# Kernel tuning notes

Measured on AMD Instinct MI355X. Metric: run time of the kernel, lower is better.

Reference implementation:

```python
import jax, jax.numpy as jnp
import numpy as np

N_NODES = 10000
N_EDGES = 4096
IN_F = 300
OUT_F = 150


def setup_inputs() -> dict:
    key = jax.random.key(0)
    ks = jax.random.split(key, 7)
    features = jax.random.normal(ks[0], (N_NODES, IN_F), dtype=jnp.float32)
    efeat = jax.random.normal(ks[1], (N_EDGES, 1), dtype=jnp.float32)
    # edge_func: Linear(1, IN_F*OUT_F) producing per-edge weight matrices
    W_edge = jax.random.normal(ks[2], (1, IN_F * OUT_F), dtype=jnp.float32) * (1.0)
    b_edge = jax.random.normal(ks[3], (IN_F * OUT_F,), dtype=jnp.float32) * 0.02
    bias = jax.random.normal(ks[4], (OUT_F,), dtype=jnp.float32) * 0.02
    src = jax.random.randint(ks[5], (N_EDGES,), 0, N_NODES, dtype=jnp.int32)
    dst = jax.random.randint(ks[6], (N_EDGES,), 0, N_NODES, dtype=jnp.int32)
    return {"features": features, "efeat": efeat, "W_edge": W_edge,
            "b_edge": b_edge, "bias": bias, "src": src, "dst": dst}


def reference(features, efeat, W_edge, b_edge, bias, src, dst):
    # edge_func: Linear on edge features -> per-edge weight matrix [E, IN_F, OUT_F]
    We = (efeat @ W_edge + b_edge).reshape(-1, IN_F, OUT_F)
    # gather source node features and apply per-edge matmul: m_e = h_src[e] @ W_e
    h_src = features[src]                       # [E, IN_F]
    msgs = jnp.einsum('ei,eio->eo', h_src, We)  # [E, OUT_F]
    # scatter-mean to destination nodes
    sums = jax.ops.segment_sum(msgs, dst, num_segments=N_NODES)          # [N, OUT_F]
    cnts = jax.ops.segment_sum(jnp.ones((msgs.shape[0],), msgs.dtype), dst,
                               num_segments=N_NODES)                     # [N]
    mean = sums / jnp.maximum(cnts, 1.0)[:, None]  # nodes w/o in-edges -> 0
    return jax.nn.relu(mean + bias)
```

## Files before the change

### kernel.cpp

```cpp
#include <hip/hip_runtime.h>

#define NNODES 10000
#define NEDGES 4096
#define INF 300
#define OUTF 150
#define EPB 16
#define NGROUPS (NEDGES / EPB)
#define SPLITK 5
#define KCHUNK (INF / SPLITK)
#define PHASES 3
#define PROWS (KCHUNK / PHASES)
#define ETHREADS 192

#define SUMS_N (NNODES * OUTF)

__global__ __launch_bounds__(ETHREADS, 4) void edge_msg_kernel(
    const float* __restrict__ feat, const float* __restrict__ efeat,
    const float* __restrict__ W, const float* __restrict__ B,
    const int* __restrict__ src, const int* __restrict__ dst,
    float* __restrict__ sums, float* __restrict__ cnts)
{
    __shared__ float hA[EPB][KCHUNK];
    __shared__ float s_ef[EPB];
    __shared__ int   s_dst[EPB];
    __shared__ int   s_src[EPB];

    const int tid = threadIdx.x;
    const int kc  = blockIdx.x / NGROUPS;
    const int grp = blockIdx.x - kc * NGROUPS;
    const int e0  = grp * EPB;
    const int k0  = kc * KCHUNK;

    if (tid < EPB) {
        const int e = e0 + tid;
        s_src[tid] = src[e];
        s_dst[tid] = dst[e];
        s_ef[tid]  = efeat[e];
    }
    __syncthreads();

    for (int q = tid; q < EPB * (KCHUNK / 4); q += ETHREADS) {
        const int el = q / (KCHUNK / 4);
        const int j4 = q - el * (KCHUNK / 4);
        *(float4*)&hA[el][4 * j4] =
            *(const float4*)(feat + (size_t)s_src[el] * INF + k0 + 4 * j4);
    }
    __syncthreads();

    if (tid < OUTF) {
        float accW[EPB], accB[EPB];
        #pragma unroll
        for (int e = 0; e < EPB; ++e) { accW[e] = 0.f; accB[e] = 0.f; }

        const float* Wc = W + (size_t)k0 * OUTF + tid;
        const float* Bc = B + (size_t)k0 * OUTF + tid;

        #pragma unroll
        for (int ph = 0; ph < PHASES; ++ph) {
            const int base = ph * PROWS;
            float wr[PROWS], br[PROWS];
            #pragma unroll
            for (int r = 0; r < PROWS; ++r) {
                wr[r] = Wc[(size_t)(base + r) * OUTF];
                br[r] = Bc[(size_t)(base + r) * OUTF];
            }
            #pragma unroll
            for (int i4 = 0; i4 < PROWS; i4 += 4) {
                #pragma unroll
                for (int e = 0; e < EPB; ++e) {
                    const float4 h = *(const float4*)&hA[e][base + i4];
                    accW[e] = fmaf(h.w, wr[i4 + 3], fmaf(h.z, wr[i4 + 2],
                              fmaf(h.y, wr[i4 + 1], fmaf(h.x, wr[i4 + 0], accW[e]))));
                    accB[e] = fmaf(h.w, br[i4 + 3], fmaf(h.z, br[i4 + 2],
                              fmaf(h.y, br[i4 + 1], fmaf(h.x, br[i4 + 0], accB[e]))));
                }
            }
        }
        #pragma unroll
        for (int e = 0; e < EPB; ++e) {
            const float msg = fmaf(s_ef[e], accW[e], accB[e]);
            atomicAdd(&sums[(size_t)s_dst[e] * OUTF + tid], msg);
        }
    } else if (kc == 0 && tid < OUTF + EPB) {
        atomicAdd(&cnts[s_dst[tid - OUTF]], 1.0f);
    }
}

__global__ __launch_bounds__(256) void finalize_kernel(
    const float* __restrict__ sums, const float* __restrict__ cnts,
    const float* __restrict__ bias, float* __restrict__ out)
{
    const int idx = blockIdx.x * blockDim.x + threadIdx.x;
    if (idx < SUMS_N) {
        const int n = idx / OUTF;
        const int o = idx - n * OUTF;
        const float c = cnts[n];
        const float m = sums[idx] / fmaxf(c, 1.0f);
        const float v = m + bias[o];
        out[idx] = v > 0.f ? v : 0.f;
    }
}

extern "C" void kernel_launch(void* const* d_in, const int* in_sizes, int n_in,
                              void* d_out, int out_size, void* d_ws, size_t ws_size,
                              hipStream_t stream) {
    const float* feat  = (const float*)d_in[0];
    const float* efeat = (const float*)d_in[1];
    const float* W     = (const float*)d_in[2];
    const float* B     = (const float*)d_in[3];
    const float* bias  = (const float*)d_in[4];
    const int*   src   = (const int*)d_in[5];
    const int*   dst   = (const int*)d_in[6];
    float* out  = (float*)d_out;

    float* sums = (float*)d_ws;
    float* cnts = sums + SUMS_N;

    hipMemsetAsync(d_ws, 0, (size_t)(SUMS_N + NNODES) * sizeof(float), stream);

    edge_msg_kernel<<<NGROUPS * SPLITK, ETHREADS, 0, stream>>>(
        feat, efeat, W, B, src, dst, sums, cnts);

    finalize_kernel<<<(SUMS_N + 255) / 256, 256, 0, stream>>>(sums, cnts, bias, out);
}
```

Measured before the change: 101.4 us.

## Write split-K partials to workspace and reduce them before atomic scatter

The edge kernel stores each split-K partial message to a workspace buffer instead of atomically adding it into node sums. A new reduce kernel adds the five partials per edge and issues one atomic per output element, cutting global atomics fivefold. A scheduling barrier is also placed between the W/B register loads and the FMA loop. The cost is an extra kernel launch plus writing and reading about 12 MB of partials.

Result: no change. 101.3 us (-0.1%).

```diff
diff --git a/kernel.cpp b/kernel.cpp
--- a/kernel.cpp
+++ b/kernel.cpp
@@ -13,16 +13,16 @@
 #define ETHREADS 192
 
 #define SUMS_N (NNODES * OUTF)
+#define MSGS_N (NEDGES * OUTF)
 
 __global__ __launch_bounds__(ETHREADS, 4) void edge_msg_kernel(
     const float* __restrict__ feat, const float* __restrict__ efeat,
     const float* __restrict__ W, const float* __restrict__ B,
-    const int* __restrict__ src, const int* __restrict__ dst,
-    float* __restrict__ sums, float* __restrict__ cnts)
+    const int* __restrict__ src,
+    float* __restrict__ part)
 {
     __shared__ float hA[EPB][KCHUNK];
     __shared__ float s_ef[EPB];
-    __shared__ int   s_dst[EPB];
     __shared__ int   s_src[EPB];
 
     const int tid = threadIdx.x;
@@ -34,7 +34,6 @@
     if (tid < EPB) {
         const int e = e0 + tid;
         s_src[tid] = src[e];
-        s_dst[tid] = dst[e];
         s_ef[tid]  = efeat[e];
     }
     __syncthreads();
@@ -64,6 +63,7 @@
                 wr[r] = Wc[(size_t)(base + r) * OUTF];
                 br[r] = Bc[(size_t)(base + r) * OUTF];
             }
+            __builtin_amdgcn_sched_barrier(0);
             #pragma unroll
             for (int i4 = 0; i4 < PROWS; i4 += 4) {
                 #pragma unroll
@@ -76,13 +76,28 @@
                 }
             }
         }
+        float* pp = part + (size_t)kc * MSGS_N + (size_t)e0 * OUTF + tid;
         #pragma unroll
-        for (int e = 0; e < EPB; ++e) {
-            const float msg = fmaf(s_ef[e], accW[e], accB[e]);
-            atomicAdd(&sums[(size_t)s_dst[e] * OUTF + tid], msg);
-        }
-    } else if (kc == 0 && tid < OUTF + EPB) {
-        atomicAdd(&cnts[s_dst[tid - OUTF]], 1.0f);
+        for (int e = 0; e < EPB; ++e)
+            pp[(size_t)e * OUTF] = fmaf(s_ef[e], accW[e], accB[e]);
+    }
+}
+
+__global__ __launch_bounds__(256) void reduce_scatter_kernel(
+    const float* __restrict__ part, const int* __restrict__ dst,
+    float* __restrict__ sums, float* __restrict__ cnts)
+{
+    const int idx = blockIdx.x * blockDim.x + threadIdx.x;
+    if (idx < MSGS_N) {
+        const int e = idx / OUTF;
+        const int o = idx - e * OUTF;
+        float s = 0.f;
+        #pragma unroll
+        for (int kc = 0; kc < SPLITK; ++kc)
+            s += part[(size_t)kc * MSGS_N + idx];
+        const int d = dst[e];
+        atomicAdd(&sums[(size_t)d * OUTF + o], s);
+        if (o == 0) atomicAdd(&cnts[d], 1.0f);
     }
 }
 
@@ -115,11 +130,15 @@
 
     float* sums = (float*)d_ws;
     float* cnts = sums + SUMS_N;
+    float* part = cnts + NNODES;
 
     hipMemsetAsync(d_ws, 0, (size_t)(SUMS_N + NNODES) * sizeof(float), stream);
 
     edge_msg_kernel<<<NGROUPS * SPLITK, ETHREADS, 0, stream>>>(
-        feat, efeat, W, B, src, dst, sums, cnts);
+        feat, efeat, W, B, src, part);
+
+    reduce_scatter_kernel<<<(MSGS_N + 255) / 256, 256, 0, stream>>>(
+        part, dst, sums, cnts);
 
     finalize_kernel<<<(SUMS_N + 255) / 256, 256, 0, stream>>>(sums, cnts, bias, out);
 }
```

## Fuse memset, edge messages and finalize into one cooperative grid-synced kernel

Applied to the files above, without the earlier changes.

Replaces the memset, edge-message kernel and finalize kernel with a single cooperative kernel that zeroes the workspace, computes and scatters messages, and applies mean+bias+ReLU, with grid.sync between stages. This aims to remove two launch gaps. It also adds a scheduling barrier after the weight-row loads to keep them grouped ahead of the FMAs. The cost is the grid-wide barrier overhead, the stricter occupancy requirement for cooperative launch (with a fallback to the old path), and a grid-stride finalize that runs on only 1280 blocks.

Measured after the change: 103.0 us. Within noise of the previous version (+1.6%).

```diff
diff --git a/kernel.cpp b/kernel.cpp
--- a/kernel.cpp
+++ b/kernel.cpp
@@ -1,4 +1,7 @@
 #include <hip/hip_runtime.h>
+#include <hip/hip_cooperative_groups.h>
+
+namespace cg = cooperative_groups;
 
 #define NNODES 10000
 #define NEDGES 4096
@@ -11,8 +14,106 @@
 #define PHASES 3
 #define PROWS (KCHUNK / PHASES)
 #define ETHREADS 192
+#define GRID (NGROUPS * SPLITK)
+#define NTHREADS (GRID * ETHREADS)
+#define NCU 256
 
 #define SUMS_N (NNODES * OUTF)
+
+__global__ __launch_bounds__(ETHREADS, 4) void fused_kernel(
+    const float* __restrict__ feat, const float* __restrict__ efeat,
+    const float* __restrict__ W, const float* __restrict__ B,
+    const float* __restrict__ bias,
+    const int* __restrict__ src, const int* __restrict__ dst,
+    float* __restrict__ sums, float* __restrict__ cnts,
+    float* __restrict__ out)
+{
+    cg::grid_group grid = cg::this_grid();
+
+    __shared__ float hA[EPB][KCHUNK];
+    __shared__ float s_ef[EPB];
+    __shared__ int   s_src[EPB];
+    __shared__ int   s_dst[EPB];
+
+    const int tid  = threadIdx.x;
+    const int gtid = blockIdx.x * ETHREADS + tid;
+
+    for (int i = gtid; i < SUMS_N + NNODES; i += NTHREADS)
+        sums[i] = 0.f;
+    grid.sync();
+
+    {
+        const int kc  = blockIdx.x / NGROUPS;
+        const int grp = blockIdx.x - kc * NGROUPS;
+        const int e0  = grp * EPB;
+        const int k0  = kc * KCHUNK;
+
+        if (tid < EPB) {
+            const int e = e0 + tid;
+            s_src[tid] = src[e];
+            s_dst[tid] = dst[e];
+            s_ef[tid]  = efeat[e];
+        }
+        __syncthreads();
+
+        for (int q = tid; q < EPB * (KCHUNK / 4); q += ETHREADS) {
+            const int el = q / (KCHUNK / 4);
+            const int j4 = q - el * (KCHUNK / 4);
+            *(float4*)&hA[el][4 * j4] =
+                *(const float4*)(feat + (size_t)s_src[el] * INF + k0 + 4 * j4);
+        }
+        __syncthreads();
+
+        if (tid < OUTF) {
+            float accW[EPB], accB[EPB];
+            #pragma unroll
+            for (int e = 0; e < EPB; ++e) { accW[e] = 0.f; accB[e] = 0.f; }
+
+            const float* Wc = W + (size_t)k0 * OUTF + tid;
+            const float* Bc = B + (size_t)k0 * OUTF + tid;
+
+            #pragma unroll
+            for (int ph = 0; ph < PHASES; ++ph) {
+                const int base = ph * PROWS;
+                float wr[PROWS], br[PROWS];
+                #pragma unroll
+                for (int r = 0; r < PROWS; ++r) {
+                    wr[r] = Wc[(size_t)(base + r) * OUTF];
+                    br[r] = Bc[(size_t)(base + r) * OUTF];
+                }
+                __builtin_amdgcn_sched_barrier(0);
+                #pragma unroll
+                for (int i4 = 0; i4 < PROWS; i4 += 4) {
+                    #pragma unroll
+                    for (int e = 0; e < EPB; ++e) {
+                        const float4 h = *(const float4*)&hA[e][base + i4];
+                        accW[e] = fmaf(h.w, wr[i4 + 3], fmaf(h.z, wr[i4 + 2],
+                                  fmaf(h.y, wr[i4 + 1], fmaf(h.x, wr[i4 + 0], accW[e]))));
+                        accB[e] = fmaf(h.w, br[i4 + 3], fmaf(h.z, br[i4 + 2],
+                                  fmaf(h.y, br[i4 + 1], fmaf(h.x, br[i4 + 0], accB[e]))));
+                    }
+                }
+            }
+            #pragma unroll
+            for (int e = 0; e < EPB; ++e) {
+                const float msg = fmaf(s_ef[e], accW[e], accB[e]);
+                atomicAdd(&sums[(size_t)s_dst[e] * OUTF + tid], msg);
+            }
+        } else if (kc == 0 && tid < OUTF + EPB) {
+            atomicAdd(&cnts[s_dst[tid - OUTF]], 1.0f);
+        }
+    }
+    grid.sync();
+
+    for (int i = gtid; i < SUMS_N; i += NTHREADS) {
+        const int n = i / OUTF;
+        const int o = i - n * OUTF;
+        const float c = cnts[n];
+        const float m = sums[i] / fmaxf(c, 1.0f);
+        const float v = m + bias[o];
+        out[i] = v > 0.f ? v : 0.f;
+    }
+}
 
 __global__ __launch_bounds__(ETHREADS, 4) void edge_msg_kernel(
     const float* __restrict__ feat, const float* __restrict__ efeat,
@@ -22,8 +123,8 @@
 {
     __shared__ float hA[EPB][KCHUNK];
     __shared__ float s_ef[EPB];
+    __shared__ int   s_src[EPB];
     __shared__ int   s_dst[EPB];
-    __shared__ int   s_src[EPB];
 
     const int tid = threadIdx.x;
     const int kc  = blockIdx.x / NGROUPS;
@@ -51,10 +152,8 @@
         float accW[EPB], accB[EPB];
         #pragma unroll
         for (int e = 0; e < EPB; ++e) { accW[e] = 0.f; accB[e] = 0.f; }
-
         const float* Wc = W + (size_t)k0 * OUTF + tid;
         const float* Bc = B + (size_t)k0 * OUTF + tid;
-
         #pragma unroll
         for (int ph = 0; ph < PHASES; ++ph) {
             const int base = ph * PROWS;
@@ -64,6 +163,7 @@
                 wr[r] = Wc[(size_t)(base + r) * OUTF];
                 br[r] = Bc[(size_t)(base + r) * OUTF];
             }
+            __builtin_amdgcn_sched_barrier(0);
             #pragma unroll
             for (int i4 = 0; i4 < PROWS; i4 += 4) {
                 #pragma unroll
@@ -116,10 +216,23 @@
     float* sums = (float*)d_ws;
     float* cnts = sums + SUMS_N;
 
-    hipMemsetAsync(d_ws, 0, (size_t)(SUMS_N + NNODES) * sizeof(float), stream);
-
-    edge_msg_kernel<<<NGROUPS * SPLITK, ETHREADS, 0, stream>>>(
-        feat, efeat, W, B, src, dst, sums, cnts);
-
-    finalize_kernel<<<(SUMS_N + 255) / 256, 256, 0, stream>>>(sums, cnts, bias, out);
-}
+    int maxBlocksPerCU = 0;
+    hipError_t err = hipOccupancyMaxActiveBlocksPerMultiprocessor(
+        &maxBlocksPerCU, (const void*)fused_kernel, ETHREADS, 0);
+
+    hipError_t launch_err = hipErrorUnknown;
+    if (err == hipSuccess && maxBlocksPerCU * NCU >= GRID) {
+        void* args[] = { (void*)&feat, (void*)&efeat, (void*)&W, (void*)&B,
+                         (void*)&bias, (void*)&src, (void*)&dst,
+                         (void*)&sums, (void*)&cnts, (void*)&out };
+        launch_err = hipLaunchCooperativeKernel((void*)fused_kernel, dim3(GRID),
+                                                dim3(ETHREADS), args, 0, stream);
+    }
+    if (launch_err != hipSuccess) {
+        hipMemsetAsync(d_ws, 0, (size_t)(SUMS_N + NNODES) * sizeof(float), stream);
+        edge_msg_kernel<<<GRID, ETHREADS, 0, stream>>>(
+            feat, efeat, W, B, src, dst, sums, cnts);
+        finalize_kernel<<<(SUMS_N + 255) / 256, 256, 0, stream>>>(
+            sums, cnts, bias, out);
+    }
+}
```
